# Kernel tuning notes

Hardware: AMD Instinct MI355X
Metric: run time of the kernel (lower is better)

## Reference

```python
import jax, jax.numpy as jnp
import numpy as np

B, L, D = 4, 2048, 1024
H, DK, DV = 16, 64, 64
EPS = 1e-6


def setup_inputs() -> dict:
    key = jax.random.key(0)
    ks = jax.random.split(key, 8)
    s = 0.02
    return {
        "q": jax.random.normal(ks[0], (B, L, D), dtype=jnp.float32),
        "k": jax.random.normal(ks[1], (B, L, D), dtype=jnp.float32),
        "v": jax.random.normal(ks[2], (B, L, D), dtype=jnp.float32),
        "Wq": jax.random.normal(ks[3], (H * DK, D), dtype=jnp.float32) * s,
        "Wk": jax.random.normal(ks[4], (H * DK, D), dtype=jnp.float32) * s,
        "Wv": jax.random.normal(ks[5], (H * DV, D), dtype=jnp.float32) * s,
        "Wfc": jax.random.normal(ks[6], (D, H * DV), dtype=jnp.float32) * s,
        "ln_g": jnp.ones((D,), dtype=jnp.float32),
        "ln_b": jnp.zeros((D,), dtype=jnp.float32),
    }


def reference(q, k, v, Wq, Wk, Wv, Wfc, ln_g, ln_b):
    residual = q
    # projections (Linear: x @ W.T), reshape to [B, H, L, d]
    qh = (q @ Wq.T).reshape(B, L, H, DK).transpose(0, 2, 1, 3)
    kh = (k @ Wk.T).reshape(B, L, H, DK).transpose(0, 2, 1, 3)
    vh = (v @ Wv.T).reshape(B, L, H, DV).transpose(0, 2, 1, 3)
    temperature = jnp.float32(DK) ** 0.5
    # scores [B, H, Lq, Lk]
    scores = jnp.einsum("bhqd,bhkd->bhqk", qh / temperature, kh)
    attn = jax.nn.softmax(scores, axis=-1)
    ctx = jnp.einsum("bhqk,bhkd->bhqd", attn, vh)  # [B, H, L, DV]
    ctx = ctx.transpose(0, 2, 1, 3).reshape(B, L, H * DV)
    out = ctx @ Wfc.T + residual
    # LayerNorm(eps=1e-6)
    mu = jnp.mean(out, axis=-1, keepdims=True)
    var = jnp.var(out, axis=-1, keepdims=True)
    out = (out - mu) * jax.lax.rsqrt(var + EPS) * ln_g + ln_b
    return out, attn
```

## Files before the change

kernel.cpp:

```cpp
#include <hip/hip_runtime.h>
#include <hip/hip_bf16.h>

typedef __bf16 bf16;
typedef __bf16 bf16x8 __attribute__((ext_vector_type(8)));
typedef __bf16 bf16x4 __attribute__((ext_vector_type(4)));
typedef float f32x4 __attribute__((ext_vector_type(4)));
typedef unsigned int u32x4 __attribute__((ext_vector_type(4)));

#define MFMA_BF16(a, b, c) __builtin_amdgcn_mfma_f32_16x16x32_bf16((a), (b), (c), 0, 0, 0)

#if defined(__has_builtin)
#if __has_builtin(__builtin_amdgcn_exp2f)
#define EXP2F(x) __builtin_amdgcn_exp2f(x)
#endif
#endif
#ifndef EXP2F
#define EXP2F(x) exp2f(x)
#endif

static constexpr int Bc = 4, Lc = 2048, Dc = 1024, Hc = 16, DKc = 64;
static constexpr int BLc = Bc * Lc;
static constexpr float CEXP = 0.18033688011112042f;

__global__ __launch_bounds__(256) void cvt_w(const float* __restrict__ src,
                                             bf16* __restrict__ dst) {
  int i = blockIdx.x * 256 + threadIdx.x;
  float4 f = ((const float4*)src)[i];
  bf16x4 o;
  o[0] = (bf16)f.x; o[1] = (bf16)f.y; o[2] = (bf16)f.z; o[3] = (bf16)f.w;
  *(bf16x4*)(dst + (size_t)i * 4) = o;
}

template <int A_F32, int OUT_F32>
__global__ __launch_bounds__(256) void gemm128(const void* __restrict__ Av,
                                               const bf16* __restrict__ Bw,
                                               void* __restrict__ Cv,
                                               const float* __restrict__ resid) {
  __shared__ bf16 As[128][72];
  __shared__ bf16 Bs[128][72];
  const int t = threadIdx.x;
  const int lane = t & 63, wid = t >> 6;
  const int wr = wid >> 1, wc = wid & 1;
  const int m0 = blockIdx.x * 128, n0 = blockIdx.y * 128;
  const int sub = t & 7, srow = t >> 3;

  f32x4 acc[4][4] = {};

  for (int kt = 0; kt < 1024; kt += 64) {
    if (A_F32) {
      const float* A = (const float*)Av;
#pragma unroll
      for (int s = 0; s < 4; ++s) {
        int r = srow + 32 * s;
        const float4* pa = (const float4*)(A + (size_t)(m0 + r) * 1024 + kt + sub * 8);
        float4 f0 = pa[0], f1 = pa[1];
        bf16x8 o;
        o[0] = (bf16)f0.x; o[1] = (bf16)f0.y; o[2] = (bf16)f0.z; o[3] = (bf16)f0.w;
        o[4] = (bf16)f1.x; o[5] = (bf16)f1.y; o[6] = (bf16)f1.z; o[7] = (bf16)f1.w;
        *(bf16x8*)&As[r][sub * 8] = o;
      }
    } else {
      const bf16* A = (const bf16*)Av;
#pragma unroll
      for (int s = 0; s < 4; ++s) {
        int r = srow + 32 * s;
        u32x4 u = *(const u32x4*)(A + (size_t)(m0 + r) * 1024 + kt + sub * 8);
        *(u32x4*)&As[r][sub * 8] = u;
      }
    }
#pragma unroll
    for (int s = 0; s < 4; ++s) {
      int r = srow + 32 * s;
      u32x4 u = *(const u32x4*)(Bw + (size_t)(n0 + r) * 1024 + kt + sub * 8);
      *(u32x4*)&Bs[r][sub * 8] = u;
    }
    __syncthreads();
#pragma unroll
    for (int c = 0; c < 2; ++c) {
      const int ko = c * 32 + (lane >> 4) * 8;
      bf16x8 af[4], bfr[4];
#pragma unroll
      for (int m = 0; m < 4; ++m)
        af[m] = *(const bf16x8*)&As[wr * 64 + m * 16 + (lane & 15)][ko];
#pragma unroll
      for (int n = 0; n < 4; ++n)
        bfr[n] = *(const bf16x8*)&Bs[wc * 64 + n * 16 + (lane & 15)][ko];
#pragma unroll
      for (int m = 0; m < 4; ++m)
#pragma unroll
        for (int n = 0; n < 4; ++n)
          acc[m][n] = MFMA_BF16(af[m], bfr[n], acc[m][n]);
    }
    __syncthreads();
  }

  const int rbase = m0 + wr * 64 + (lane >> 4) * 4;
  const int cbase = n0 + wc * 64 + (lane & 15);
  if (OUT_F32) {
    float* C = (float*)Cv;
#pragma unroll
    for (int m = 0; m < 4; ++m)
#pragma unroll
      for (int n = 0; n < 4; ++n)
#pragma unroll
        for (int r = 0; r < 4; ++r) {
          size_t row = (size_t)(rbase + m * 16 + r);
          size_t col = (size_t)(cbase + n * 16);
          C[row * 1024 + col] = acc[m][n][r] + resid[row * 1024 + col];
        }
  } else {
    bf16* C = (bf16*)Cv;
#pragma unroll
    for (int m = 0; m < 4; ++m)
#pragma unroll
      for (int n = 0; n < 4; ++n)
#pragma unroll
        for (int r = 0; r < 4; ++r) {
          size_t row = (size_t)(rbase + m * 16 + r);
          size_t col = (size_t)(cbase + n * 16);
          C[row * 1024 + col] = (bf16)acc[m][n][r];
        }
  }
}

__global__ __launch_bounds__(256) void attn_kernel(const bf16* __restrict__ qh,
                                                   const bf16* __restrict__ kh,
                                                   const bf16* __restrict__ vh,
                                                   bf16* __restrict__ ctx,
                                                   float* __restrict__ attn_out) {
  __shared__ bf16 Ks[64][72];
  __shared__ bf16 Vt[64][72];
  __shared__ bf16 Ps[4][16][72];
  const int t = threadIdx.x, lane = t & 63, w = t >> 6;
  const int qt = blockIdx.x, h = blockIdx.y, b = blockIdx.z;
  const size_t rowbase = (size_t)b * 2048;
  const bf16* qbase = qh + (rowbase + qt * 64) * 1024 + h * 64;
  const bf16* kbase = kh + rowbase * 1024 + h * 64;
  const bf16* vbase = vh + rowbase * 1024 + h * 64;
  const int sub = t & 7, srow = t >> 3;

  bf16x8 qf[2];
  {
    const bf16* qr = qbase + (size_t)(w * 16 + (lane & 15)) * 1024 + (lane >> 4) * 8;
    qf[0] = *(const bf16x8*)(qr);
    qf[1] = *(const bf16x8*)(qr + 32);
  }

  f32x4 cacc[4] = {};
  float zacc[4] = {0.f, 0.f, 0.f, 0.f};

  for (int kt = 0; kt < 2048; kt += 64) {
#pragma unroll
    for (int s = 0; s < 2; ++s) {
      int r = srow + 32 * s;
      u32x4 u = *(const u32x4*)(kbase + (size_t)(kt + r) * 1024 + sub * 8);
      *(u32x4*)&Ks[r][sub * 8] = u;
    }
#pragma unroll
    for (int s = 0; s < 2; ++s) {
      int r = srow + 32 * s;
      u32x4 u = *(const u32x4*)(vbase + (size_t)(kt + r) * 1024 + sub * 8);
      bf16x8 x = __builtin_bit_cast(bf16x8, u);
#pragma unroll
      for (int j = 0; j < 8; ++j) Vt[sub * 8 + j][r] = x[j];
    }
    __syncthreads();

    f32x4 s4[4] = {};
#pragma unroll
    for (int c = 0; c < 2; ++c) {
      const int ko = c * 32 + (lane >> 4) * 8;
#pragma unroll
      for (int n = 0; n < 4; ++n) {
        bf16x8 kf = *(const bf16x8*)&Ks[n * 16 + (lane & 15)][ko];
        s4[n] = MFMA_BF16(qf[c], kf, s4[n]);
      }
    }
#pragma unroll
    for (int n = 0; n < 4; ++n)
#pragma unroll
      for (int r = 0; r < 4; ++r) {
        float p = EXP2F(s4[n][r] * CEXP);
        zacc[r] += p;
        Ps[w][(lane >> 4) * 4 + r][n * 16 + (lane & 15)] = (bf16)p;
      }
#pragma unroll
    for (int c = 0; c < 2; ++c) {
      const int ko = c * 32 + (lane >> 4) * 8;
      bf16x8 pf = *(const bf16x8*)&Ps[w][lane & 15][ko];
#pragma unroll
      for (int n = 0; n < 4; ++n) {
        bf16x8 vf = *(const bf16x8*)&Vt[n * 16 + (lane & 15)][ko];
        cacc[n] = MFMA_BF16(pf, vf, cacc[n]);
      }
    }
    __syncthreads();
  }

#pragma unroll
  for (int r = 0; r < 4; ++r) {
    float z = zacc[r];
    z += __shfl_xor(z, 1);
    z += __shfl_xor(z, 2);
    z += __shfl_xor(z, 4);
    z += __shfl_xor(z, 8);
    zacc[r] = 1.0f / z;
  }
  {
    size_t row0 = rowbase + qt * 64 + w * 16 + (lane >> 4) * 4;
    int col0 = h * 64 + (lane & 15);
#pragma unroll
    for (int n = 0; n < 4; ++n)
#pragma unroll
      for (int r = 0; r < 4; ++r)
        ctx[(row0 + r) * 1024 + col0 + n * 16] = (bf16)(cacc[n][r] * zacc[r]);
  }

  float* abase = attn_out +
      ((size_t)(b * 16 + h) * 2048 + qt * 64 + w * 16 + (lane >> 4) * 4) * 2048;
  for (int kt = 0; kt < 2048; kt += 64) {
    __syncthreads();
#pragma unroll
    for (int s = 0; s < 2; ++s) {
      int r = srow + 32 * s;
      u32x4 u = *(const u32x4*)(kbase + (size_t)(kt + r) * 1024 + sub * 8);
      *(u32x4*)&Ks[r][sub * 8] = u;
    }
    __syncthreads();
    f32x4 s4[4] = {};
#pragma unroll
    for (int c = 0; c < 2; ++c) {
      const int ko = c * 32 + (lane >> 4) * 8;
#pragma unroll
      for (int n = 0; n < 4; ++n) {
        bf16x8 kf = *(const bf16x8*)&Ks[n * 16 + (lane & 15)][ko];
        s4[n] = MFMA_BF16(qf[c], kf, s4[n]);
      }
    }
#pragma unroll
    for (int n = 0; n < 4; ++n)
#pragma unroll
      for (int r = 0; r < 4; ++r)
        abase[(size_t)r * 2048 + kt + n * 16 + (lane & 15)] =
            EXP2F(s4[n][r] * CEXP) * zacc[r];
  }
}

__global__ __launch_bounds__(256) void ln_kernel(float* __restrict__ io,
                                                 const float* __restrict__ g,
                                                 const float* __restrict__ bta) {
  const int row = blockIdx.x, t = threadIdx.x;
  float4* rp = (float4*)(io + (size_t)row * 1024);
  float4 v = rp[t];
  float s = v.x + v.y + v.z + v.w;
  float s2 = v.x * v.x + v.y * v.y + v.z * v.z + v.w * v.w;
#pragma unroll
  for (int off = 32; off >= 1; off >>= 1) {
    s += __shfl_xor(s, off);
    s2 += __shfl_xor(s2, off);
  }
  __shared__ float ls[4], ls2[4];
  const int w = t >> 6;
  if ((t & 63) == 0) { ls[w] = s; ls2[w] = s2; }
  __syncthreads();
  s = ls[0] + ls[1] + ls[2] + ls[3];
  s2 = ls2[0] + ls2[1] + ls2[2] + ls2[3];
  float mu = s * (1.f / 1024.f);
  float var = s2 * (1.f / 1024.f) - mu * mu;
  float rs = rsqrtf(var + 1e-6f);
  float4 gv = ((const float4*)g)[t];
  float4 bv = ((const float4*)bta)[t];
  v.x = (v.x - mu) * rs * gv.x + bv.x;
  v.y = (v.y - mu) * rs * gv.y + bv.y;
  v.z = (v.z - mu) * rs * gv.z + bv.z;
  v.w = (v.w - mu) * rs * gv.w + bv.w;
  rp[t] = v;
}

extern "C" void kernel_launch(void* const* d_in, const int* in_sizes, int n_in,
                              void* d_out, int out_size, void* d_ws, size_t ws_size,
                              hipStream_t stream) {
  (void)in_sizes; (void)n_in; (void)out_size; (void)ws_size;
  const float* q    = (const float*)d_in[0];
  const float* k    = (const float*)d_in[1];
  const float* v    = (const float*)d_in[2];
  const float* Wq   = (const float*)d_in[3];
  const float* Wk   = (const float*)d_in[4];
  const float* Wv   = (const float*)d_in[5];
  const float* Wfc  = (const float*)d_in[6];
  const float* ln_g = (const float*)d_in[7];
  const float* ln_b = (const float*)d_in[8];

  char* ws = (char*)d_ws;
  const size_t MB = 1024ull * 1024ull;
  bf16* wqb  = (bf16*)(ws + 0 * MB);
  bf16* wkb  = (bf16*)(ws + 2 * MB);
  bf16* wvb  = (bf16*)(ws + 4 * MB);
  bf16* wfcb = (bf16*)(ws + 6 * MB);
  bf16* qh   = (bf16*)(ws + 8 * MB);
  bf16* kh   = (bf16*)(ws + 24 * MB);
  bf16* vh   = (bf16*)(ws + 40 * MB);
  bf16* ctx  = (bf16*)(ws + 56 * MB);

  float* outp  = (float*)d_out;
  float* attnp = outp + (size_t)BLc * Dc;

  cvt_w<<<1024, 256, 0, stream>>>(Wq, wqb);
  cvt_w<<<1024, 256, 0, stream>>>(Wk, wkb);
  cvt_w<<<1024, 256, 0, stream>>>(Wv, wvb);
  cvt_w<<<1024, 256, 0, stream>>>(Wfc, wfcb);

  dim3 gg(64, 8);
  gemm128<1, 0><<<gg, 256, 0, stream>>>(q, wqb, qh, nullptr);
  gemm128<1, 0><<<gg, 256, 0, stream>>>(k, wkb, kh, nullptr);
  gemm128<1, 0><<<gg, 256, 0, stream>>>(v, wvb, vh, nullptr);

  attn_kernel<<<dim3(32, 16, 4), 256, 0, stream>>>(qh, kh, vh, ctx, attnp);

  gemm128<0, 1><<<gg, 256, 0, stream>>>(ctx, wfcb, outp, q);
  ln_kernel<<<8192, 256, 0, stream>>>(outp, ln_g, ln_b);
}
```

Measured before the change: 575.4 us.

## Switch attention to 32x32 MFMA, pre-transpose V in GEMM epilogue, keep P in registers

The V projection GEMM now writes V transposed per (batch, head), so the attention kernel loads V into LDS with plain vector copies instead of a scalar transpose. Attention now uses 32x32x16 MFMA with 128 query rows per block. The exponentiated score tile is repacked into A-operand layout through cross-lane shuffles rather than a round trip through shared memory. The second pass that writes the attention matrix reads K straight from global memory with no LDS staging or barriers, and stores float4 vectors. In exchange, the V GEMM epilogue does strided scattered stores, and the grid has half as many blocks.

```diff
diff --git a/kernel.cpp b/kernel.cpp
--- a/kernel.cpp
+++ b/kernel.cpp
@@ -4,10 +4,13 @@
 typedef __bf16 bf16;
 typedef __bf16 bf16x8 __attribute__((ext_vector_type(8)));
 typedef __bf16 bf16x4 __attribute__((ext_vector_type(4)));
+typedef __bf16 bf16x2 __attribute__((ext_vector_type(2)));
 typedef float f32x4 __attribute__((ext_vector_type(4)));
+typedef float f32x16 __attribute__((ext_vector_type(16)));
 typedef unsigned int u32x4 __attribute__((ext_vector_type(4)));
 
 #define MFMA_BF16(a, b, c) __builtin_amdgcn_mfma_f32_16x16x32_bf16((a), (b), (c), 0, 0, 0)
+#define MFMA32(a, b, c) __builtin_amdgcn_mfma_f32_32x32x16_bf16((a), (b), (c), 0, 0, 0)
 
 #if defined(__has_builtin)
 #if __has_builtin(__builtin_amdgcn_exp2f)
@@ -22,6 +25,13 @@
 static constexpr int BLc = Bc * Lc;
 static constexpr float CEXP = 0.18033688011112042f;
 
+__device__ inline unsigned pk2(float a, float b) {
+  bf16x2 t;
+  t[0] = (bf16)a;
+  t[1] = (bf16)b;
+  return __builtin_bit_cast(unsigned, t);
+}
+
 __global__ __launch_bounds__(256) void cvt_w(const float* __restrict__ src,
                                              bf16* __restrict__ dst) {
   int i = blockIdx.x * 256 + threadIdx.x;
@@ -31,7 +41,7 @@
   *(bf16x4*)(dst + (size_t)i * 4) = o;
 }
 
-template <int A_F32, int OUT_F32>
+template <int A_F32, int OUT_MODE>
 __global__ __launch_bounds__(256) void gemm128(const void* __restrict__ Av,
                                                const bf16* __restrict__ Bw,
                                                void* __restrict__ Cv,
@@ -96,7 +106,7 @@
 
   const int rbase = m0 + wr * 64 + (lane >> 4) * 4;
   const int cbase = n0 + wc * 64 + (lane & 15);
-  if (OUT_F32) {
+  if (OUT_MODE == 1) {
     float* C = (float*)Cv;
 #pragma unroll
     for (int m = 0; m < 4; ++m)
@@ -108,7 +118,7 @@
           size_t col = (size_t)(cbase + n * 16);
           C[row * 1024 + col] = acc[m][n][r] + resid[row * 1024 + col];
         }
-  } else {
+  } else if (OUT_MODE == 0) {
     bf16* C = (bf16*)Cv;
 #pragma unroll
     for (int m = 0; m < 4; ++m)
@@ -120,129 +130,141 @@
           size_t col = (size_t)(cbase + n * 16);
           C[row * 1024 + col] = (bf16)acc[m][n][r];
         }
-  }
-}
-
-__global__ __launch_bounds__(256) void attn_kernel(const bf16* __restrict__ qh,
-                                                   const bf16* __restrict__ kh,
-                                                   const bf16* __restrict__ vh,
-                                                   bf16* __restrict__ ctx,
-                                                   float* __restrict__ attn_out) {
+  } else {
+    bf16* C = (bf16*)Cv;
+#pragma unroll
+    for (int m = 0; m < 4; ++m)
+#pragma unroll
+      for (int n = 0; n < 4; ++n)
+#pragma unroll
+        for (int r = 0; r < 4; ++r) {
+          int row = rbase + m * 16 + r;
+          int col = cbase + n * 16;
+          size_t dst = ((size_t)((row >> 11) << 10) + col) * 2048 + (row & 2047);
+          C[dst] = (bf16)acc[m][n][r];
+        }
+  }
+}
+
+__global__ __launch_bounds__(256, 3) void attn_kernel(const bf16* __restrict__ qh,
+                                                      const bf16* __restrict__ kh,
+                                                      const bf16* __restrict__ vt,
+                                                      bf16* __restrict__ ctx,
+                                                      float* __restrict__ attn_out) {
   __shared__ bf16 Ks[64][72];
-  __shared__ bf16 Vt[64][72];
-  __shared__ bf16 Ps[4][16][72];
+  __shared__ bf16 Vs[64][72];
   const int t = threadIdx.x, lane = t & 63, w = t >> 6;
+  const int hi = lane >> 5, ql = lane & 31;
   const int qt = blockIdx.x, h = blockIdx.y, b = blockIdx.z;
   const size_t rowbase = (size_t)b * 2048;
-  const bf16* qbase = qh + (rowbase + qt * 64) * 1024 + h * 64;
+  const int qrow = qt * 128 + w * 32 + ql;
   const bf16* kbase = kh + rowbase * 1024 + h * 64;
-  const bf16* vbase = vh + rowbase * 1024 + h * 64;
+  const bf16* vbase = vt + (size_t)(b * 16 + h) * 64 * 2048;
   const int sub = t & 7, srow = t >> 3;
 
-  bf16x8 qf[2];
+  bf16x8 qf[4];
   {
-    const bf16* qr = qbase + (size_t)(w * 16 + (lane & 15)) * 1024 + (lane >> 4) * 8;
-    qf[0] = *(const bf16x8*)(qr);
-    qf[1] = *(const bf16x8*)(qr + 32);
-  }
-
-  f32x4 cacc[4] = {};
-  float zacc[4] = {0.f, 0.f, 0.f, 0.f};
+    const bf16* qp = qh + (rowbase + qrow) * 1024 + h * 64 + hi * 8;
+#pragma unroll
+    for (int c = 0; c < 4; ++c) qf[c] = *(const bf16x8*)(qp + c * 16);
+  }
+
+  f32x16 cacc[2] = {};
+  float zacc = 0.f;
 
   for (int kt = 0; kt < 2048; kt += 64) {
+    __syncthreads();
 #pragma unroll
     for (int s = 0; s < 2; ++s) {
       int r = srow + 32 * s;
-      u32x4 u = *(const u32x4*)(kbase + (size_t)(kt + r) * 1024 + sub * 8);
-      *(u32x4*)&Ks[r][sub * 8] = u;
-    }
-#pragma unroll
-    for (int s = 0; s < 2; ++s) {
-      int r = srow + 32 * s;
-      u32x4 u = *(const u32x4*)(vbase + (size_t)(kt + r) * 1024 + sub * 8);
-      bf16x8 x = __builtin_bit_cast(bf16x8, u);
-#pragma unroll
-      for (int j = 0; j < 8; ++j) Vt[sub * 8 + j][r] = x[j];
+      *(u32x4*)&Ks[r][sub * 8] =
+          *(const u32x4*)(kbase + (size_t)(kt + r) * 1024 + sub * 8);
+      *(u32x4*)&Vs[r][sub * 8] =
+          *(const u32x4*)(vbase + (size_t)r * 2048 + kt + sub * 8);
     }
     __syncthreads();
-
-    f32x4 s4[4] = {};
-#pragma unroll
-    for (int c = 0; c < 2; ++c) {
-      const int ko = c * 32 + (lane >> 4) * 8;
-#pragma unroll
-      for (int n = 0; n < 4; ++n) {
-        bf16x8 kf = *(const bf16x8*)&Ks[n * 16 + (lane & 15)][ko];
-        s4[n] = MFMA_BF16(qf[c], kf, s4[n]);
-      }
-    }
-#pragma unroll
-    for (int n = 0; n < 4; ++n)
-#pragma unroll
-      for (int r = 0; r < 4; ++r) {
-        float p = EXP2F(s4[n][r] * CEXP);
-        zacc[r] += p;
-        Ps[w][(lane >> 4) * 4 + r][n * 16 + (lane & 15)] = (bf16)p;
-      }
-#pragma unroll
-    for (int c = 0; c < 2; ++c) {
-      const int ko = c * 32 + (lane >> 4) * 8;
-      bf16x8 pf = *(const bf16x8*)&Ps[w][lane & 15][ko];
-#pragma unroll
-      for (int n = 0; n < 4; ++n) {
-        bf16x8 vf = *(const bf16x8*)&Vt[n * 16 + (lane & 15)][ko];
-        cacc[n] = MFMA_BF16(pf, vf, cacc[n]);
-      }
-    }
-    __syncthreads();
-  }
-
-#pragma unroll
-  for (int r = 0; r < 4; ++r) {
-    float z = zacc[r];
-    z += __shfl_xor(z, 1);
-    z += __shfl_xor(z, 2);
-    z += __shfl_xor(z, 4);
-    z += __shfl_xor(z, 8);
-    zacc[r] = 1.0f / z;
-  }
+#pragma unroll
+    for (int sb = 0; sb < 2; ++sb) {
+      f32x16 s = {};
+#pragma unroll
+      for (int c = 0; c < 4; ++c) {
+        bf16x8 kf = *(const bf16x8*)&Ks[sb * 32 + ql][c * 16 + hi * 8];
+        s = MFMA32(kf, qf[c], s);
+      }
+      float p[16];
+#pragma unroll
+      for (int j = 0; j < 16; ++j) {
+        p[j] = EXP2F(s[j] * CEXP);
+        zacc += p[j];
+      }
+      unsigned pv[4][2];
+#pragma unroll
+      for (int o = 0; o < 4; ++o)
+#pragma unroll
+        for (int d = 0; d < 2; ++d) pv[o][d] = pk2(p[o * 4 + 2 * d], p[o * 4 + 2 * d + 1]);
+      bf16x8 pa[2];
+#pragma unroll
+      for (int c = 0; c < 2; ++c) {
+        u32x4 pu;
+#pragma unroll
+        for (int d = 0; d < 2; ++d) {
+          unsigned a = pv[2 * c][d], bq = pv[2 * c + 1][d];
+          unsigned as = (unsigned)__shfl_xor((int)a, 32);
+          unsigned bs = (unsigned)__shfl_xor((int)bq, 32);
+          pu[d] = hi ? bs : a;
+          pu[2 + d] = hi ? bq : as;
+        }
+        pa[c] = __builtin_bit_cast(bf16x8, pu);
+      }
+#pragma unroll
+      for (int n = 0; n < 2; ++n)
+#pragma unroll
+        for (int c = 0; c < 2; ++c) {
+          bf16x8 vf = *(const bf16x8*)&Vs[n * 32 + ql][sb * 32 + c * 16 + hi * 8];
+          cacc[n] = MFMA32(pa[c], vf, cacc[n]);
+        }
+    }
+  }
+
+  float z = zacc + __shfl_xor(zacc, 32);
+  float rz = 1.0f / z;
+
   {
-    size_t row0 = rowbase + qt * 64 + w * 16 + (lane >> 4) * 4;
-    int col0 = h * 64 + (lane & 15);
-#pragma unroll
-    for (int n = 0; n < 4; ++n)
-#pragma unroll
-      for (int r = 0; r < 4; ++r)
-        ctx[(row0 + r) * 1024 + col0 + n * 16] = (bf16)(cacc[n][r] * zacc[r]);
-  }
-
-  float* abase = attn_out +
-      ((size_t)(b * 16 + h) * 2048 + qt * 64 + w * 16 + (lane >> 4) * 4) * 2048;
+    float rzv[16];
+#pragma unroll
+    for (int g = 0; g < 16; ++g)
+      rzv[g] = __shfl(rz, (g & 3) + 8 * (g >> 2) + 4 * hi);
+#pragma unroll
+    for (int n = 0; n < 2; ++n)
+#pragma unroll
+      for (int g = 0; g < 16; ++g) {
+        int crow = (g & 3) + 8 * (g >> 2) + 4 * hi;
+        size_t row = rowbase + (size_t)(qt * 128 + w * 32 + crow);
+        ctx[row * 1024 + h * 64 + n * 32 + ql] = (bf16)(cacc[n][g] * rzv[g]);
+      }
+  }
+
+  float* abase = attn_out + ((size_t)(b * 16 + h) * 2048 + qrow) * 2048;
   for (int kt = 0; kt < 2048; kt += 64) {
-    __syncthreads();
-#pragma unroll
-    for (int s = 0; s < 2; ++s) {
-      int r = srow + 32 * s;
-      u32x4 u = *(const u32x4*)(kbase + (size_t)(kt + r) * 1024 + sub * 8);
-      *(u32x4*)&Ks[r][sub * 8] = u;
-    }
-    __syncthreads();
-    f32x4 s4[4] = {};
-#pragma unroll
-    for (int c = 0; c < 2; ++c) {
-      const int ko = c * 32 + (lane >> 4) * 8;
-#pragma unroll
-      for (int n = 0; n < 4; ++n) {
-        bf16x8 kf = *(const bf16x8*)&Ks[n * 16 + (lane & 15)][ko];
-        s4[n] = MFMA_BF16(qf[c], kf, s4[n]);
-      }
-    }
-#pragma unroll
-    for (int n = 0; n < 4; ++n)
-#pragma unroll
-      for (int r = 0; r < 4; ++r)
-        abase[(size_t)r * 2048 + kt + n * 16 + (lane & 15)] =
-            EXP2F(s4[n][r] * CEXP) * zacc[r];
+#pragma unroll
+    for (int sb = 0; sb < 2; ++sb) {
+      f32x16 s = {};
+      const bf16* kp = kbase + (size_t)(kt + sb * 32 + ql) * 1024 + hi * 8;
+#pragma unroll
+      for (int c = 0; c < 4; ++c) {
+        bf16x8 kf = *(const bf16x8*)(kp + c * 16);
+        s = MFMA32(kf, qf[c], s);
+      }
+#pragma unroll
+      for (int o = 0; o < 4; ++o) {
+        float4 v4;
+        v4.x = EXP2F(s[o * 4 + 0] * CEXP) * rz;
+        v4.y = EXP2F(s[o * 4 + 1] * CEXP) * rz;
+        v4.z = EXP2F(s[o * 4 + 2] * CEXP) * rz;
+        v4.w = EXP2F(s[o * 4 + 3] * CEXP) * rz;
+        *(float4*)(abase + kt + sb * 32 + o * 8 + hi * 4) = v4;
+      }
+    }
   }
 }
 
@@ -299,7 +321,7 @@
   bf16* wfcb = (bf16*)(ws + 6 * MB);
   bf16* qh   = (bf16*)(ws + 8 * MB);
   bf16* kh   = (bf16*)(ws + 24 * MB);
-  bf16* vh   = (bf16*)(ws + 40 * MB);
+  bf16* vt   = (bf16*)(ws + 40 * MB);
   bf16* ctx  = (bf16*)(ws + 56 * MB);
 
   float* outp  = (float*)d_out;
@@ -313,9 +335,9 @@
   dim3 gg(64, 8);
   gemm128<1, 0><<<gg, 256, 0, stream>>>(q, wqb, qh, nullptr);
   gemm128<1, 0><<<gg, 256, 0, stream>>>(k, wkb, kh, nullptr);
-  gemm128<1, 0><<<gg, 256, 0, stream>>>(v, wvb, vh, nullptr);
-
-  attn_kernel<<<dim3(32, 16, 4), 256, 0, stream>>>(qh, kh, vh, ctx, attnp);
+  gemm128<1, 2><<<gg, 256, 0, stream>>>(v, wvb, vt, nullptr);
+
+  attn_kernel<<<dim3(16, 16, 4), 256, 0, stream>>>(qh, kh, vt, ctx, attnp);
 
   gemm128<0, 1><<<gg, 256, 0, stream>>>(ctx, wfcb, outp, q);
   ln_kernel<<<8192, 256, 0, stream>>>(outp, ln_g, ln_b);
```

Result: slower. 596.0 us (+3.6%).

## Double-buffer projection GEMMs with direct global-to-LDS loads and 128x256 tiles

Applied to the files above, without the earlier changes.

Replaces the 128x128 projection GEMM with a 128x256-tile, 512-thread kernel. The next K-slice is prefetched into a second LDS buffer while MFMAs run on the current one. The B operand (and the bf16 A operand) goes straight to LDS via global_load_lds with an XOR swizzle instead of padded rows, and fp32 A is register-prefetched and converted after compute. This aims to hide global load latency and cut bank conflicts and sync count, at the cost of more LDS per block (96 KB), which limits how many blocks fit on each CU.

```diff
diff --git a/kernel.cpp b/kernel.cpp
--- a/kernel.cpp
+++ b/kernel.cpp
@@ -22,6 +22,12 @@
 static constexpr int BLc = Bc * Lc;
 static constexpr float CEXP = 0.18033688011112042f;
 
+__device__ __forceinline__ void gload_lds16(const bf16* g, bf16* l) {
+  __builtin_amdgcn_global_load_lds(
+      (const __attribute__((address_space(1))) void*)g,
+      (__attribute__((address_space(3))) void*)l, 16, 0, 0);
+}
+
 __global__ __launch_bounds__(256) void cvt_w(const float* __restrict__ src,
                                              bf16* __restrict__ dst) {
   int i = blockIdx.x * 256 + threadIdx.x;
@@ -32,67 +38,117 @@
 }
 
 template <int A_F32, int OUT_F32>
-__global__ __launch_bounds__(256) void gemm128(const void* __restrict__ Av,
-                                               const bf16* __restrict__ Bw,
-                                               void* __restrict__ Cv,
-                                               const float* __restrict__ resid) {
-  __shared__ bf16 As[128][72];
-  __shared__ bf16 Bs[128][72];
+__global__ __launch_bounds__(512, 2) void gemm256(const void* __restrict__ Av,
+                                                  const bf16* __restrict__ Bw,
+                                                  void* __restrict__ Cv,
+                                                  const float* __restrict__ resid) {
+  __shared__ bf16 As[2][128 * 64];
+  __shared__ bf16 Bs[2][256 * 64];
   const int t = threadIdx.x;
   const int lane = t & 63, wid = t >> 6;
-  const int wr = wid >> 1, wc = wid & 1;
-  const int m0 = blockIdx.x * 128, n0 = blockIdx.y * 128;
-  const int sub = t & 7, srow = t >> 3;
+  const int wr = wid >> 2, wc = wid & 3;
+  const int m0 = blockIdx.x * 128, n0 = blockIdx.y * 256;
+  const float* Af = (const float*)Av;
+  const bf16* Ab = (const bf16*)Av;
+  const int arow = t >> 2, aseg = t & 3;
 
   f32x4 acc[4][4] = {};
-
+  float4 fr0, fr1, fr2, fr3;
+
+#define STAGE_B(buf, kt)                                                        \
+  {                                                                             \
+    _Pragma("unroll") for (int cc = 0; cc < 4; ++cc) {                          \
+      int chunk = wid + cc * 8;                                      \
+      int row = chunk * 8 + (lane >> 3);                            \
+      int scol = ((lane & 7) ^ (row & 7)) * 8;                                  \
+      gload_lds16(Bw + (size_t)(n0 + row) * 1024 + (kt) + scol,                 \
+                  &Bs[buf][chunk * 512 + lane * 8]);                            \
+    }                                                                           \
+  }
+
+#define STAGE_A_LDS(buf, kt)                                                    \
+  {                                                                             \
+    _Pragma("unroll") for (int cc = 0; cc < 2; ++cc) {                          \
+      int chunk = wid + cc * 8;                                      \
+      int row = chunk * 8 + (lane >> 3);                            \
+      int scol = ((lane & 7) ^ (row & 7)) * 8;                                  \
+      gload_lds16(Ab + (size_t)(m0 + row) * 1024 + (kt) + scol,                 \
+                  &As[buf][chunk * 512 + lane * 8]);                            \
+    }                                                                           \
+  }
+
+#define LOAD_A(kt)                                                              \
+  {                                                                             \
+    const float* ap = Af + (size_t)(m0 + arow) * 1024 + (kt) + aseg * 16;       \
+    fr0 = ((const float4*)ap)[0];                                               \
+    fr1 = ((const float4*)ap)[1];                                               \
+    fr2 = ((const float4*)ap)[2];                                               \
+    fr3 = ((const float4*)ap)[3];                                               \
+  }
+
+#define WRITE_A(buf)                                                            \
+  {                                                                             \
+    bf16x8 o0, o1;                                                              \
+    o0[0] = (bf16)fr0.x; o0[1] = (bf16)fr0.y; o0[2] = (bf16)fr0.z;              \
+    o0[3] = (bf16)fr0.w; o0[4] = (bf16)fr1.x; o0[5] = (bf16)fr1.y;              \
+    o0[6] = (bf16)fr1.z; o0[7] = (bf16)fr1.w;                                   \
+    o1[0] = (bf16)fr2.x; o1[1] = (bf16)fr2.y; o1[2] = (bf16)fr2.z;              \
+    o1[3] = (bf16)fr2.w; o1[4] = (bf16)fr3.x; o1[5] = (bf16)fr3.y;              \
+    o1[6] = (bf16)fr3.z; o1[7] = (bf16)fr3.w;                                   \
+    int s0 = ((aseg * 2) ^ (arow & 7)) * 8;                                     \
+    int s1 = ((aseg * 2 + 1) ^ (arow & 7)) * 8;                                 \
+    *(bf16x8*)&As[buf][arow * 64 + s0] = o0;                                    \
+    *(bf16x8*)&As[buf][arow * 64 + s1] = o1;                                    \
+  }
+
+  if (A_F32) { LOAD_A(0); }
+  STAGE_B(0, 0);
+  if (!A_F32) { STAGE_A_LDS(0, 0); }
+  if (A_F32) { WRITE_A(0); }
+  asm volatile("s_waitcnt vmcnt(0)" ::: "memory");
+  __syncthreads();
+
+  int buf = 0;
   for (int kt = 0; kt < 1024; kt += 64) {
-    if (A_F32) {
-      const float* A = (const float*)Av;
-#pragma unroll
-      for (int s = 0; s < 4; ++s) {
-        int r = srow + 32 * s;
-        const float4* pa = (const float4*)(A + (size_t)(m0 + r) * 1024 + kt + sub * 8);
-        float4 f0 = pa[0], f1 = pa[1];
-        bf16x8 o;
-        o[0] = (bf16)f0.x; o[1] = (bf16)f0.y; o[2] = (bf16)f0.z; o[3] = (bf16)f0.w;
-        o[4] = (bf16)f1.x; o[5] = (bf16)f1.y; o[6] = (bf16)f1.z; o[7] = (bf16)f1.w;
-        *(bf16x8*)&As[r][sub * 8] = o;
-      }
-    } else {
-      const bf16* A = (const bf16*)Av;
-#pragma unroll
-      for (int s = 0; s < 4; ++s) {
-        int r = srow + 32 * s;
-        u32x4 u = *(const u32x4*)(A + (size_t)(m0 + r) * 1024 + kt + sub * 8);
-        *(u32x4*)&As[r][sub * 8] = u;
-      }
-    }
-#pragma unroll
-    for (int s = 0; s < 4; ++s) {
-      int r = srow + 32 * s;
-      u32x4 u = *(const u32x4*)(Bw + (size_t)(n0 + r) * 1024 + kt + sub * 8);
-      *(u32x4*)&Bs[r][sub * 8] = u;
-    }
-    __syncthreads();
+    const bool notlast = kt < 960;
+    if (notlast) {
+      if (A_F32) { LOAD_A(kt + 64); }
+      STAGE_B(buf ^ 1, kt + 64);
+      if (!A_F32) { STAGE_A_LDS(buf ^ 1, kt + 64); }
+    }
 #pragma unroll
     for (int c = 0; c < 2; ++c) {
-      const int ko = c * 32 + (lane >> 4) * 8;
+      const int slot = c * 4 + (lane >> 4);
       bf16x8 af[4], bfr[4];
 #pragma unroll
-      for (int m = 0; m < 4; ++m)
-        af[m] = *(const bf16x8*)&As[wr * 64 + m * 16 + (lane & 15)][ko];
-#pragma unroll
-      for (int n = 0; n < 4; ++n)
-        bfr[n] = *(const bf16x8*)&Bs[wc * 64 + n * 16 + (lane & 15)][ko];
+      for (int m = 0; m < 4; ++m) {
+        int row = wr * 64 + m * 16 + (lane & 15);
+        af[m] = *(const bf16x8*)((const char*)&As[buf][0] + row * 128 +
+                                 ((slot ^ (row & 7)) * 16));
+      }
+#pragma unroll
+      for (int n = 0; n < 4; ++n) {
+        int row = wc * 64 + n * 16 + (lane & 15);
+        bfr[n] = *(const bf16x8*)((const char*)&Bs[buf][0] + row * 128 +
+                                  ((slot ^ (row & 7)) * 16));
+      }
 #pragma unroll
       for (int m = 0; m < 4; ++m)
 #pragma unroll
         for (int n = 0; n < 4; ++n)
           acc[m][n] = MFMA_BF16(af[m], bfr[n], acc[m][n]);
     }
-    __syncthreads();
-  }
+    if (notlast) {
+      if (A_F32) { WRITE_A(buf ^ 1); }
+      asm volatile("s_waitcnt vmcnt(0)" ::: "memory");
+      __syncthreads();
+      buf ^= 1;
+    }
+  }
+#undef STAGE_B
+#undef STAGE_A_LDS
+#undef LOAD_A
+#undef WRITE_A
 
   const int rbase = m0 + wr * 64 + (lane >> 4) * 4;
   const int cbase = n0 + wc * 64 + (lane & 15);
@@ -310,13 +366,13 @@
   cvt_w<<<1024, 256, 0, stream>>>(Wv, wvb);
   cvt_w<<<1024, 256, 0, stream>>>(Wfc, wfcb);
 
-  dim3 gg(64, 8);
-  gemm128<1, 0><<<gg, 256, 0, stream>>>(q, wqb, qh, nullptr);
-  gemm128<1, 0><<<gg, 256, 0, stream>>>(k, wkb, kh, nullptr);
-  gemm128<1, 0><<<gg, 256, 0, stream>>>(v, wvb, vh, nullptr);
+  dim3 gg(64, 4);
+  gemm256<1, 0><<<gg, 512, 0, stream>>>(q, wqb, qh, nullptr);
+  gemm256<1, 0><<<gg, 512, 0, stream>>>(k, wkb, kh, nullptr);
+  gemm256<1, 0><<<gg, 512, 0, stream>>>(v, wvb, vh, nullptr);
 
   attn_kernel<<<dim3(32, 16, 4), 256, 0, stream>>>(qh, kh, vh, ctx, attnp);
 
-  gemm128<0, 1><<<gg, 256, 0, stream>>>(ctx, wfcb, outp, q);
+  gemm256<0, 1><<<gg, 512, 0, stream>>>(ctx, wfcb, outp, q);
   ln_kernel<<<8192, 256, 0, stream>>>(outp, ln_g, ln_b);
 }
```

After: 590.0 us. 1.03x slower.

## Use direct global-to-LDS loads with XOR swizzle; read K directly in attn-prob pass

Applied to the files above, without the earlier changes.

The GEMM kernel now stages B tiles (and bf16 A tiles) with global_load_lds into an unpadded LDS layout that is XOR-swizzled to avoid bank conflicts. The fp32 A path writes into the same swizzle. The second attention pass, which writes the probabilities, drops its LDS staging of K and both barriers and reads K fragments straight from global memory. The four weight conversions are merged into one launch. The costs are uncoalesced global K reads in the attention loop and the extra alignment requirements of direct LDS loads.

```diff
diff --git a/kernel.cpp b/kernel.cpp
--- a/kernel.cpp
+++ b/kernel.cpp
@@ -22,69 +22,88 @@
 static constexpr int BLc = Bc * Lc;
 static constexpr float CEXP = 0.18033688011112042f;
 
-__global__ __launch_bounds__(256) void cvt_w(const float* __restrict__ src,
-                                             bf16* __restrict__ dst) {
-  int i = blockIdx.x * 256 + threadIdx.x;
-  float4 f = ((const float4*)src)[i];
-  bf16x4 o;
-  o[0] = (bf16)f.x; o[1] = (bf16)f.y; o[2] = (bf16)f.z; o[3] = (bf16)f.w;
-  *(bf16x4*)(dst + (size_t)i * 4) = o;
+__device__ __forceinline__ void gload_lds16(const bf16* g, bf16* l) {
+  __builtin_amdgcn_global_load_lds(
+      (const __attribute__((address_space(1))) void*)g,
+      (__attribute__((address_space(3))) void*)l, 16, 0, 0);
+}
+
+__global__ __launch_bounds__(256) void cvt_all(const float* __restrict__ s0,
+                                               const float* __restrict__ s1,
+                                               const float* __restrict__ s2,
+                                               const float* __restrict__ s3,
+                                               bf16* __restrict__ dst) {
+  size_t i = ((size_t)blockIdx.x * 256 + threadIdx.x) * 8;
+  const float* srcs[4] = {s0, s1, s2, s3};
+  const float* sp = srcs[i >> 20] + (i & 1048575);
+  float4 f0 = ((const float4*)sp)[0];
+  float4 f1 = ((const float4*)sp)[1];
+  bf16x8 o;
+  o[0] = (bf16)f0.x; o[1] = (bf16)f0.y; o[2] = (bf16)f0.z; o[3] = (bf16)f0.w;
+  o[4] = (bf16)f1.x; o[5] = (bf16)f1.y; o[6] = (bf16)f1.z; o[7] = (bf16)f1.w;
+  *(bf16x8*)(dst + i) = o;
 }
 
 template <int A_F32, int OUT_F32>
-__global__ __launch_bounds__(256) void gemm128(const void* __restrict__ Av,
-                                               const bf16* __restrict__ Bw,
-                                               void* __restrict__ Cv,
-                                               const float* __restrict__ resid) {
-  __shared__ bf16 As[128][72];
-  __shared__ bf16 Bs[128][72];
+__global__ __launch_bounds__(256) void gemm128s(const void* __restrict__ Av,
+                                                const bf16* __restrict__ Bw,
+                                                void* __restrict__ Cv,
+                                                const float* __restrict__ resid) {
+  __shared__ bf16 As[128 * 64];
+  __shared__ bf16 Bs[128 * 64];
   const int t = threadIdx.x;
   const int lane = t & 63, wid = t >> 6;
   const int wr = wid >> 1, wc = wid & 1;
   const int m0 = blockIdx.x * 128, n0 = blockIdx.y * 128;
-  const int sub = t & 7, srow = t >> 3;
 
   f32x4 acc[4][4] = {};
 
   for (int kt = 0; kt < 1024; kt += 64) {
+#pragma unroll
+    for (int cgl = 0; cgl < 4; ++cgl) {
+      int idx = cgl * 256 + t;
+      int row = idx >> 3, slot = idx & 7;
+      int scol = (slot ^ (row & 7)) * 8;
+      gload_lds16(Bw + (size_t)(n0 + row) * 1024 + kt + scol, Bs + idx * 8);
+    }
     if (A_F32) {
       const float* A = (const float*)Av;
+      const int sub = t & 7, srow0 = t >> 3;
 #pragma unroll
       for (int s = 0; s < 4; ++s) {
-        int r = srow + 32 * s;
-        const float4* pa = (const float4*)(A + (size_t)(m0 + r) * 1024 + kt + sub * 8);
+        int row = srow0 + 32 * s;
+        const float4* pa = (const float4*)(A + (size_t)(m0 + row) * 1024 + kt + sub * 8);
         float4 f0 = pa[0], f1 = pa[1];
         bf16x8 o;
         o[0] = (bf16)f0.x; o[1] = (bf16)f0.y; o[2] = (bf16)f0.z; o[3] = (bf16)f0.w;
         o[4] = (bf16)f1.x; o[5] = (bf16)f1.y; o[6] = (bf16)f1.z; o[7] = (bf16)f1.w;
-        *(bf16x8*)&As[r][sub * 8] = o;
+        *(bf16x8*)&As[row * 64 + ((sub ^ (row & 7)) * 8)] = o;
       }
     } else {
       const bf16* A = (const bf16*)Av;
 #pragma unroll
-      for (int s = 0; s < 4; ++s) {
-        int r = srow + 32 * s;
-        u32x4 u = *(const u32x4*)(A + (size_t)(m0 + r) * 1024 + kt + sub * 8);
-        *(u32x4*)&As[r][sub * 8] = u;
-      }
-    }
-#pragma unroll
-    for (int s = 0; s < 4; ++s) {
-      int r = srow + 32 * s;
-      u32x4 u = *(const u32x4*)(Bw + (size_t)(n0 + r) * 1024 + kt + sub * 8);
-      *(u32x4*)&Bs[r][sub * 8] = u;
+      for (int cgl = 0; cgl < 4; ++cgl) {
+        int idx = cgl * 256 + t;
+        int row = idx >> 3, slot = idx & 7;
+        int scol = (slot ^ (row & 7)) * 8;
+        gload_lds16(A + (size_t)(m0 + row) * 1024 + kt + scol, As + idx * 8);
+      }
     }
     __syncthreads();
 #pragma unroll
     for (int c = 0; c < 2; ++c) {
-      const int ko = c * 32 + (lane >> 4) * 8;
+      const int slot = c * 4 + (lane >> 4);
       bf16x8 af[4], bfr[4];
 #pragma unroll
-      for (int m = 0; m < 4; ++m)
-        af[m] = *(const bf16x8*)&As[wr * 64 + m * 16 + (lane & 15)][ko];
-#pragma unroll
-      for (int n = 0; n < 4; ++n)
-        bfr[n] = *(const bf16x8*)&Bs[wc * 64 + n * 16 + (lane & 15)][ko];
+      for (int m = 0; m < 4; ++m) {
+        int row = wr * 64 + m * 16 + (lane & 15);
+        af[m] = *(const bf16x8*)&As[row * 64 + ((slot ^ (row & 7)) * 8)];
+      }
+#pragma unroll
+      for (int n = 0; n < 4; ++n) {
+        int row = wc * 64 + n * 16 + (lane & 15);
+        bfr[n] = *(const bf16x8*)&Bs[row * 64 + ((slot ^ (row & 7)) * 8)];
+      }
 #pragma unroll
       for (int m = 0; m < 4; ++m)
 #pragma unroll
@@ -219,21 +238,14 @@
   float* abase = attn_out +
       ((size_t)(b * 16 + h) * 2048 + qt * 64 + w * 16 + (lane >> 4) * 4) * 2048;
   for (int kt = 0; kt < 2048; kt += 64) {
-    __syncthreads();
-#pragma unroll
-    for (int s = 0; s < 2; ++s) {
-      int r = srow + 32 * s;
-      u32x4 u = *(const u32x4*)(kbase + (size_t)(kt + r) * 1024 + sub * 8);
-      *(u32x4*)&Ks[r][sub * 8] = u;
-    }
-    __syncthreads();
     f32x4 s4[4] = {};
 #pragma unroll
     for (int c = 0; c < 2; ++c) {
       const int ko = c * 32 + (lane >> 4) * 8;
 #pragma unroll
       for (int n = 0; n < 4; ++n) {
-        bf16x8 kf = *(const bf16x8*)&Ks[n * 16 + (lane & 15)][ko];
+        bf16x8 kf =
+            *(const bf16x8*)(kbase + (size_t)(kt + n * 16 + (lane & 15)) * 1024 + ko);
         s4[n] = MFMA_BF16(qf[c], kf, s4[n]);
       }
     }
@@ -305,18 +317,15 @@
   float* outp  = (float*)d_out;
   float* attnp = outp + (size_t)BLc * Dc;
 
-  cvt_w<<<1024, 256, 0, stream>>>(Wq, wqb);
-  cvt_w<<<1024, 256, 0, stream>>>(Wk, wkb);
-  cvt_w<<<1024, 256, 0, stream>>>(Wv, wvb);
-  cvt_w<<<1024, 256, 0, stream>>>(Wfc, wfcb);
+  cvt_all<<<2048, 256, 0, stream>>>(Wq, Wk, Wv, Wfc, wqb);
 
   dim3 gg(64, 8);
-  gemm128<1, 0><<<gg, 256, 0, stream>>>(q, wqb, qh, nullptr);
-  gemm128<1, 0><<<gg, 256, 0, stream>>>(k, wkb, kh, nullptr);
-  gemm128<1, 0><<<gg, 256, 0, stream>>>(v, wvb, vh, nullptr);
+  gemm128s<1, 0><<<gg, 256, 0, stream>>>(q, wqb, qh, nullptr);
+  gemm128s<1, 0><<<gg, 256, 0, stream>>>(k, wkb, kh, nullptr);
+  gemm128s<1, 0><<<gg, 256, 0, stream>>>(v, wvb, vh, nullptr);
 
   attn_kernel<<<dim3(32, 16, 4), 256, 0, stream>>>(qh, kh, vh, ctx, attnp);
 
-  gemm128<0, 1><<<gg, 256, 0, stream>>>(ctx, wfcb, outp, q);
+  gemm128s<0, 1><<<gg, 256, 0, stream>>>(ctx, wfcb, outp, q);
   ln_kernel<<<8192, 256, 0, stream>>>(outp, ln_g, ln_b);
 }
```

Measured after the change: 671.2 us. 16.7% more time.
